# Kernel optimization log

Measured on AMD Instinct MI355X. Metric: run time of the kernel, lower is better.

## Reference

```python
import jax, jax.numpy as jnp
import numpy as np

TAU_M = 2.0   # membrane time constant
TAU_S = 1.0   # synaptic time constant (tau_m = 2*tau_s -> closed-form spike times)
THETA = 1.0   # firing threshold
T_MAX = 20.0  # times beyond this count as 'no spike' (inf)
EPS = 1e-6


def lif_forward(input_spike_times, input_spike_synapse_ids, Wff, Wrec, max_output_spikes):
    """Event-driven recurrent LIF solver.

    PSP kernel: w * (exp(-(t-ts)/TAU_M) - exp(-(t-ts)/TAU_S)).
    Membrane: V(t) = A*z - B*z^2 with z = exp(-t/TAU_M), where A, B accumulate
    w*exp(ts/TAU_M) and w*exp(ts/TAU_S) per processed event. Spike when V = THETA
    (quadratic in z). Reset-by-subtraction of THETA via the membrane kernel.
    Emitted spikes are re-injected through the recurrent weights as new events.
    """
    Bsz, S = input_spike_times.shape
    N = Wff.shape[0]
    M = int(max_output_spikes)
    # process input events in causal (time) order
    order = jnp.argsort(input_spike_times, axis=1)
    t_srt = jnp.take_along_axis(input_spike_times, order, axis=1)
    sid_srt = jnp.take_along_axis(input_spike_synapse_ids, order, axis=1)
    bidx = jnp.arange(Bsz)
    WffT = Wff.T   # (n_synapses, N): row s = weights from synapse s to all neurons
    WrecT = Wrec.T # (N, N): row j = weights from neuron j to all neurons

    def step(carry, _):
        A, Bacc, ptr, t_cur, out_t, out_id, cnt = carry
        ptr_c = jnp.clip(ptr, 0, S - 1)
        t_in = jnp.where(ptr < S, t_srt[bidx, ptr_c], jnp.inf)  # next input event
        sid = sid_srt[bidx, ptr_c]
        # next threshold crossing per neuron: solve A z - B z^2 = THETA
        disc = A * A - 4.0 * THETA * Bacc
        ok_d = (disc > 0.0) & (Bacc > 1e-12)
        sq = jnp.sqrt(jnp.where(ok_d, disc, 1.0))
        Bs = jnp.where(Bacc > 1e-12, Bacc, 1.0)
        z_cur = jnp.exp(-t_cur / TAU_M)[:, None]

        def root_time(z):
            ok = ok_d & (z > 1e-12) & (z < z_cur * (1.0 - EPS))  # strictly in the future
            zs = jnp.where(ok, z, 0.5)
            return jnp.where(ok, -TAU_M * jnp.log(zs), jnp.inf)

        t1 = root_time((A - sq) / (2.0 * Bs))
        t2 = root_time((A + sq) / (2.0 * Bs))
        t_cand = jnp.minimum(t1, t2)                      # (B, N)
        j = jnp.argmin(t_cand, axis=1)                    # earliest-spiking neuron
        t_spk = t_cand[bidx, j]
        emit = (t_spk < t_in) & (t_spk < T_MAX) & (cnt < M)
        consume = (~emit) & jnp.isfinite(t_in)
        any_ev = emit | consume
        t_ev = jnp.where(emit, t_spk, t_in)
        t_evs = jnp.where(any_ev, t_ev, 0.0)
        em = jnp.exp(t_evs / TAU_M)[:, None]
        es = jnp.exp(t_evs / TAU_S)[:, None]
        w_in = WffT[sid]   # (B, N)
        w_rec = WrecT[j]   # (B, N)
        reset = THETA * jax.nn.one_hot(j, N, dtype=A.dtype)
        dA = jnp.where(consume[:, None], w_in * em, 0.0) + jnp.where(emit[:, None], (w_rec - reset) * em, 0.0)
        dB = jnp.where(consume[:, None], w_in * es, 0.0) + jnp.where(emit[:, None], w_rec * es, 0.0)
        A = A + dA
        Bacc = Bacc + dB
        ptr = ptr + consume.astype(ptr.dtype)
        t_cur = jnp.where(any_ev, t_ev, t_cur)
        slot = jnp.clip(cnt, 0, M - 1)
        out_t = out_t.at[bidx, slot].set(jnp.where(emit, t_spk, out_t[bidx, slot]))
        out_id = out_id.at[bidx, slot].set(jnp.where(emit, j.astype(out_id.dtype), out_id[bidx, slot]))
        cnt = cnt + emit.astype(cnt.dtype)
        return (A, Bacc, ptr, t_cur, out_t, out_id, cnt), None

    init = (
        jnp.zeros((Bsz, N), jnp.float32),
        jnp.zeros((Bsz, N), jnp.float32),
        jnp.zeros((Bsz,), jnp.int32),
        jnp.zeros((Bsz,), jnp.float32),
        jnp.full((Bsz, M), jnp.inf, jnp.float32),
        jnp.full((Bsz, M), -1, jnp.int32),
        jnp.zeros((Bsz,), jnp.int32),
    )
    carry, _ = jax.lax.scan(step, init, None, length=S + M)
    return carry[4], carry[5]


def setup_inputs() -> dict:
    key = jax.random.key(0)
    k1, k2, k3, k4 = jax.random.split(key, 4)
    batch, max_in, n_neurons, n_synapses = 256, 256, 128, 256
    input_spike_times = jax.random.uniform(k1, (batch, max_in), dtype=jnp.float32)
    input_spike_synapse_ids = jax.random.randint(k2, (batch, max_in), 0, n_synapses, dtype=jnp.int32)
    # module init: randn + 1.0, rescaled so the membrane operates near threshold
    feedforward_weights = (jax.random.normal(k3, (n_neurons, n_synapses), jnp.float32) + 1.0) * (4.0 / n_synapses)
    recurrent_weights = (jax.random.normal(k4, (n_neurons, n_neurons), jnp.float32) + 1.0) * (1.0 / n_neurons)
    return {
        "input_spike_times": input_spike_times,
        "input_spike_synapse_ids": input_spike_synapse_ids,
        "feedforward_weights": feedforward_weights,
        "recurrent_weights": recurrent_weights,
        "max_output_spikes": 256,
    }


def reference(input_spike_times, input_spike_synapse_ids, feedforward_weights, recurrent_weights, max_output_spikes):
    return lif_forward(input_spike_times, input_spike_synapse_ids, feedforward_weights, recurrent_weights, max_output_spikes)
```

## Files before the change

### kernel.cpp

```cpp
#include <hip/hip_runtime.h>

namespace {

constexpr int BATCH = 256;
constexpr int S_IN  = 256;
constexpr int NNEUR = 128;
constexpr int NSYN  = 256;
constexpr int MOUT  = 256;
constexpr int WSTR  = 130;
constexpr float NO_SPIKE_T = 1.0e30f;
constexpr float K1  = 0.72134752044448170f;
constexpr float NL2 = -1.3862943611198906f;
constexpr float ZEPS = (float)(1.0 - 1e-6);
constexpr float Z20F = 4.5399929762484854e-05f;

constexpr int LDS_WREC  = NNEUR * WSTR * 4;
constexpr int LDS_EV    = LDS_WREC;
constexpr int LDS_SPK   = LDS_EV + 264 * 16;
constexpr int LDS_LT    = LDS_SPK + 264 * 4;
constexpr int LDS_TOTAL = LDS_LT + 1024;

__device__ __forceinline__ float hw_exp2(float x) { return __builtin_amdgcn_exp2f(x); }
__device__ __forceinline__ float hw_log2(float x) { return __builtin_amdgcn_logf(x); }
__device__ __forceinline__ float hw_rcp(float x)  { return __builtin_amdgcn_rcpf(x); }

__global__ void transpose_wff_kernel(const float* __restrict__ wff,
                                     float* __restrict__ wffT) {
    int i = blockIdx.x * blockDim.x + threadIdx.x;
    int s = i >> 7;
    int n = i & (NNEUR - 1);
    wffT[i] = wff[n * NSYN + s];
}

template <int CTRL>
__device__ __forceinline__ int dpp_imax(int v) {
    int t = __builtin_amdgcn_update_dpp(v, v, CTRL, 0xf, 0xf, false);
    return (t > v) ? t : v;
}

__device__ __forceinline__ float cand_z(float A, float B, float zlim) {
    float disc = __builtin_fmaf(A, A, -4.0f * B);
    float r2B  = hw_rcp(B + B);
    float sq   = __fsqrt_rn(disc);
    float z2 = (A + sq) * r2B;
    float z1 = (A - sq) * r2B;
    bool okd = (disc > 0.0f) & (B > 1e-12f);
    bool v2 = okd & (z2 > 1e-12f) & (z2 < zlim);
    bool v1 = okd & (z1 > 1e-12f) & (z1 < zlim);
    return v2 ? z2 : (v1 ? z1 : 0.0f);
}

__global__ __launch_bounds__(64, 1) void lif_event_kernel(
    const float* __restrict__ in_t,
    const int*   __restrict__ in_sid,
    const float* __restrict__ wff,
    const float* __restrict__ wffT,
    const float* __restrict__ wrec,
    int use_t,
    float* __restrict__ out_t,
    float* __restrict__ out_id)
{
    extern __shared__ char smem[];
    float*  wrecL = (float*)smem;
    float4* evL   = (float4*)(smem + LDS_EV);
    int*    spkI  = (int*)  (smem + LDS_SPK);
    float*  lt    = (float*)(smem + LDS_LT);

    const int b = blockIdx.x;
    const int lane = threadIdx.x;

    const float4* wrec4 = (const float4*)wrec;
    for (int i = lane; i < NNEUR * NNEUR / 4; i += 64) {
        float4 v = wrec4[i];
        int n  = i >> 5;
        int c0 = (i & 31) * 4;
        wrecL[(c0 + 0) * WSTR + n] = v.x;
        wrecL[(c0 + 1) * WSTR + n] = v.y;
        wrecL[(c0 + 2) * WSTR + n] = v.z;
        wrecL[(c0 + 3) * WSTR + n] = v.w;
    }

    float myt[4]; int mys[4];
    for (int q = 0; q < 4; ++q) {
        int k = lane + 64 * q;
        myt[q] = in_t[b * S_IN + k];
        mys[q] = in_sid[b * S_IN + k];
        lt[k] = myt[q];
    }
    __syncthreads();
    int rk[4] = {0, 0, 0, 0};
    for (int j = 0; j < S_IN; ++j) {
        float tj = lt[j];
        #pragma unroll
        for (int q = 0; q < 4; ++q)
            rk[q] += (tj < myt[q] || (tj == myt[q] && j < lane + 64 * q)) ? 1 : 0;
    }
    for (int q = 0; q < 4; ++q) {
        float t = myt[q];
        float zi = hw_exp2(-K1 * t);
        float e  = hw_exp2(K1 * t);
        evL[rk[q]] = make_float4(__builtin_bit_cast(float, mys[q]), zi, e, e * e);
    }
    if (lane < 8) evL[S_IN + lane] = make_float4(0.0f, 0.0f, 1.0f, 1.0f);
    __syncthreads();

    const int n0 = lane * 2;
    const int n1 = n0 + 1;
    const int KZ20 = __builtin_bit_cast(int, Z20F) & ~127;

    float A0 = 0.f, A1 = 0.f, B0 = 0.f, B1 = 0.f;
    int ptr = 0, cnt = 0;
    float zlim = ZEPS;

#define LOADW(dst, sid_)                                                     \
    do {                                                                     \
        const int s_ = (sid_);                                               \
        if (use_t) dst = *(const float2*)&wffT[s_ * NNEUR + n0];             \
        else       dst = make_float2(wff[n0 * NSYN + s_], wff[n1 * NSYN + s_]); \
    } while (0)

#define REDUCE_KEY(kk, zc, idxl)                                             \
    do {                                                                     \
        int key_ = (__builtin_bit_cast(int, (zc)) & ~127) | (127 - (idxl));  \
        key_ = dpp_imax<0x111>(key_);                                        \
        key_ = dpp_imax<0x112>(key_);                                        \
        key_ = dpp_imax<0x114>(key_);                                        \
        key_ = dpp_imax<0x118>(key_);                                        \
        key_ = dpp_imax<0x142>(key_);                                        \
        key_ = dpp_imax<0x143>(key_);                                        \
        kk = __builtin_amdgcn_readlane(key_, 63);                            \
    } while (0)

#define APPLY_EMIT(kk)                                                       \
    do {                                                                     \
        const int jn_ = 127 - ((kk) & 127);                                  \
        const float zmax_ = __builtin_bit_cast(float, (kk) & ~127);          \
        const float2 wr_ = *(const float2*)&wrecL[jn_ * WSTR + n0];          \
        const float em_ = hw_rcp(zmax_);                                     \
        const float es_ = em_ * em_;                                         \
        const float r0_ = (n0 == jn_) ? 1.0f : 0.0f;                         \
        const float r1_ = (n1 == jn_) ? 1.0f : 0.0f;                         \
        A0 = __builtin_fmaf(wr_.x - r0_, em_, A0);                           \
        A1 = __builtin_fmaf(wr_.y - r1_, em_, A1);                           \
        B0 = __builtin_fmaf(wr_.x, es_, B0);                                 \
        B1 = __builtin_fmaf(wr_.y, es_, B1);                                 \
        zlim = ZEPS * zmax_;                                                 \
    } while (0)

    float4 evA = evL[0], evB = evL[1], evC = evL[2], evD = evL[3];
    float2 wA, wB, wC, wD;
    LOADW(wA, __builtin_bit_cast(int, evA.x));
    LOADW(wB, __builtin_bit_cast(int, evB.x));
    LOADW(wC, __builtin_bit_cast(int, evC.x));
    LOADW(wD, __builtin_bit_cast(int, evD.x));

    while (ptr + 4 <= S_IN && cnt < MOUT) {
        const float zb0 = cand_z(A0, B0, zlim);
        const float zb1 = cand_z(A1, B1, zlim);
        const float zc = fmaxf(zb0, zb1);
        const int idxl = (zb1 > zb0) ? n1 : n0;
        int key;
        REDUCE_KEY(key, zc, idxl);

        const float A0p = __builtin_fmaf(wA.x, evA.z, A0);
        const float A1p = __builtin_fmaf(wA.y, evA.z, A1);
        const float B0p = __builtin_fmaf(wA.x, evA.w, B0);
        const float B1p = __builtin_fmaf(wA.y, evA.w, B1);
        const float zl1 = ZEPS * evA.y;
        const float zc1 = fmaxf(cand_z(A0p, B0p, zl1), cand_z(A1p, B1p, zl1));

        const float A0q = __builtin_fmaf(wB.x, evB.z, A0p);
        const float A1q = __builtin_fmaf(wB.y, evB.z, A1p);
        const float B0q = __builtin_fmaf(wB.x, evB.w, B0p);
        const float B1q = __builtin_fmaf(wB.y, evB.w, B1p);
        const float zl2 = ZEPS * evB.y;
        const float zc2 = fmaxf(cand_z(A0q, B0q, zl2), cand_z(A1q, B1q, zl2));

        const float A0r = __builtin_fmaf(wC.x, evC.z, A0q);
        const float A1r = __builtin_fmaf(wC.y, evC.z, A1q);
        const float B0r = __builtin_fmaf(wC.x, evC.w, B0q);
        const float B1r = __builtin_fmaf(wC.y, evC.w, B1q);
        const float zl3 = ZEPS * evC.y;
        const float zc3 = fmaxf(cand_z(A0r, B0r, zl3), cand_z(A1r, B1r, zl3));

        const unsigned long long m0 = __ballot((zc  > evA.y) & (zc  > Z20F));
        const unsigned long long m1 = __ballot((zc1 > evB.y) & (zc1 > Z20F));
        const unsigned long long m2 = __ballot((zc2 > evC.y) & (zc2 > Z20F));
        const unsigned long long m3 = __ballot((zc3 > evD.y) & (zc3 > Z20F));

        if (m0 != 0ull) {
            APPLY_EMIT(key);
            if (lane == 0) spkI[cnt] = key;
            ++cnt;
        } else if (m1 != 0ull) {
            A0 = A0p; A1 = A1p; B0 = B0p; B1 = B1p; zlim = zl1; ptr += 1;
            evA = evB; evB = evC; evC = evD; wA = wB; wB = wC; wC = wD;
            evD = evL[ptr + 3];
            LOADW(wD, __builtin_bit_cast(int, evD.x));
        } else if (m2 != 0ull) {
            A0 = A0q; A1 = A1q; B0 = B0q; B1 = B1q; zlim = zl2; ptr += 2;
            evA = evC; evB = evD; wA = wC; wB = wD;
            evC = evL[ptr + 2]; evD = evL[ptr + 3];
            LOADW(wC, __builtin_bit_cast(int, evC.x));
            LOADW(wD, __builtin_bit_cast(int, evD.x));
        } else if (m3 != 0ull) {
            A0 = A0r; A1 = A1r; B0 = B0r; B1 = B1r; zlim = zl3; ptr += 3;
            evA = evD; wA = wD;
            evB = evL[ptr + 1]; evC = evL[ptr + 2]; evD = evL[ptr + 3];
            LOADW(wB, __builtin_bit_cast(int, evB.x));
            LOADW(wC, __builtin_bit_cast(int, evC.x));
            LOADW(wD, __builtin_bit_cast(int, evD.x));
        } else {
            A0 = __builtin_fmaf(wD.x, evD.z, A0r);
            A1 = __builtin_fmaf(wD.y, evD.z, A1r);
            B0 = __builtin_fmaf(wD.x, evD.w, B0r);
            B1 = __builtin_fmaf(wD.y, evD.w, B1r);
            zlim = ZEPS * evD.y; ptr += 4;
            evA = evL[ptr + 0]; evB = evL[ptr + 1];
            evC = evL[ptr + 2]; evD = evL[ptr + 3];
            LOADW(wA, __builtin_bit_cast(int, evA.x));
            LOADW(wB, __builtin_bit_cast(int, evB.x));
            LOADW(wC, __builtin_bit_cast(int, evC.x));
            LOADW(wD, __builtin_bit_cast(int, evD.x));
        }
    }

    while (ptr < S_IN && cnt < MOUT) {
        const float zb0 = cand_z(A0, B0, zlim);
        const float zb1 = cand_z(A1, B1, zlim);
        const float zc = fmaxf(zb0, zb1);
        const int idxl = (zb1 > zb0) ? n1 : n0;
        int key;
        REDUCE_KEY(key, zc, idxl);
        const unsigned long long m = __ballot((zc > evA.y) & (zc > Z20F));
        if (m != 0ull) {
            APPLY_EMIT(key);
            if (lane == 0) spkI[cnt] = key;
            ++cnt;
        } else {
            A0 = __builtin_fmaf(wA.x, evA.z, A0);
            A1 = __builtin_fmaf(wA.y, evA.z, A1);
            B0 = __builtin_fmaf(wA.x, evA.w, B0);
            B1 = __builtin_fmaf(wA.y, evA.w, B1);
            zlim = ZEPS * evA.y;
            ++ptr;
            evA = evB; evB = evC; evC = evD; wA = wB; wB = wC; wC = wD;
            evD = evL[ptr + 3];
            LOADW(wD, __builtin_bit_cast(int, evD.x));
        }
    }

    while (cnt < MOUT) {
        int k0, k1, k2, k3;
        {
            const float zb0 = cand_z(A0, B0, zlim);
            const float zb1 = cand_z(A1, B1, zlim);
            const float zc = fmaxf(zb0, zb1);
            const int idxl = (zb1 > zb0) ? n1 : n0;
            REDUCE_KEY(k0, zc, idxl);
            APPLY_EMIT(k0);
        }
        {
            const float zb0 = cand_z(A0, B0, zlim);
            const float zb1 = cand_z(A1, B1, zlim);
            const float zc = fmaxf(zb0, zb1);
            const int idxl = (zb1 > zb0) ? n1 : n0;
            REDUCE_KEY(k1, zc, idxl);
            APPLY_EMIT(k1);
        }
        {
            const float zb0 = cand_z(A0, B0, zlim);
            const float zb1 = cand_z(A1, B1, zlim);
            const float zc = fmaxf(zb0, zb1);
            const int idxl = (zb1 > zb0) ? n1 : n0;
            REDUCE_KEY(k2, zc, idxl);
            APPLY_EMIT(k2);
        }
        {
            const float zb0 = cand_z(A0, B0, zlim);
            const float zb1 = cand_z(A1, B1, zlim);
            const float zc = fmaxf(zb0, zb1);
            const int idxl = (zb1 > zb0) ? n1 : n0;
            REDUCE_KEY(k3, zc, idxl);
            APPLY_EMIT(k3);
        }
        if (lane == 0) {
            spkI[cnt + 0] = k0; spkI[cnt + 1] = k1;
            spkI[cnt + 2] = k2; spkI[cnt + 3] = k3;
        }
        const bool f0 = (k0 & ~127) <= KZ20;
        const bool f1 = (k1 & ~127) <= KZ20;
        const bool f2 = (k2 & ~127) <= KZ20;
        const bool f3 = (k3 & ~127) <= KZ20;
        const int p = f0 ? 0 : (f1 ? 1 : (f2 ? 2 : (f3 ? 3 : 4)));
        cnt += p;
        if (p < 4) break;
    }
    if (cnt > MOUT) cnt = MOUT;
#undef LOADW
#undef REDUCE_KEY
#undef APPLY_EMIT

    __syncthreads();
    for (int k = lane; k < MOUT; k += 64) {
        const int kk = spkI[k];
        const bool live = (k < cnt);
        const float zmax = __builtin_bit_cast(float, kk & ~127);
        const float t = NL2 * hw_log2(zmax);
        const float id = (float)(127 - (kk & 127));
        out_t[b * MOUT + k]  = live ? t : NO_SPIKE_T;
        out_id[b * MOUT + k] = live ? id : -1.0f;
    }
}

}

extern "C" void kernel_launch(void* const* d_in, const int* in_sizes, int n_in,
                              void* d_out, int out_size, void* d_ws, size_t ws_size,
                              hipStream_t stream) {
    (void)in_sizes; (void)n_in; (void)out_size;
    const float* in_t   = (const float*)d_in[0];
    const int*   in_sid = (const int*)d_in[1];
    const float* wff    = (const float*)d_in[2];
    const float* wrec   = (const float*)d_in[3];

    float* out_t  = (float*)d_out;
    float* out_id = (float*)d_out + BATCH * MOUT;

    float* wffT = (float*)d_ws;
    const size_t need = (size_t)(NSYN * NNEUR) * sizeof(float);
    const int use_t = (ws_size >= need) ? 1 : 0;

    if (use_t) {
        transpose_wff_kernel<<<(NSYN * NNEUR) / 256, 256, 0, stream>>>(wff, wffT);
    }
    lif_event_kernel<<<BATCH, 64, LDS_TOTAL, stream>>>(in_t, in_sid, wff, wffT, wrec,
                                                       use_t, out_t, out_id);
}
```

Before: 163.5 us.

## Pre-bake reset into recurrent weight layout, deepen weight prefetch, unroll emit loop

Stores recurrent weights in LDS as one float4 per lane (reset-adjusted A weights plus B weights), indexed directly by the reduced key, so each emit does a single 16-byte LDS read and no per-neuron reset compare. A separate synapse-id array lets feedforward weight loads be issued eight events ahead instead of four. The key reduction folds both neurons without an extra index select, and the tail emit loop is unrolled to eight steps. LDS use grows to roughly 135 KB and register pressure rises. es is now computed with a second reciprocal, which may differ slightly in rounding from squaring em.

```diff
diff --git a/kernel.cpp b/kernel.cpp
--- a/kernel.cpp
+++ b/kernel.cpp
@@ -7,17 +7,17 @@
 constexpr int NNEUR = 128;
 constexpr int NSYN  = 256;
 constexpr int MOUT  = 256;
-constexpr int WSTR  = 130;
 constexpr float NO_SPIKE_T = 1.0e30f;
 constexpr float K1  = 0.72134752044448170f;
 constexpr float NL2 = -1.3862943611198906f;
 constexpr float ZEPS = (float)(1.0 - 1e-6);
 constexpr float Z20F = 4.5399929762484854e-05f;
 
-constexpr int LDS_WREC  = NNEUR * WSTR * 4;
-constexpr int LDS_EV    = LDS_WREC;
-constexpr int LDS_SPK   = LDS_EV + 264 * 16;
-constexpr int LDS_LT    = LDS_SPK + 264 * 4;
+constexpr int LDS_WR4   = 0;
+constexpr int LDS_EV    = 131072;
+constexpr int LDS_SPK   = LDS_EV + 4224;
+constexpr int LDS_SS    = LDS_SPK + 1056;
+constexpr int LDS_LT    = LDS_SS + 1088;
 constexpr int LDS_TOTAL = LDS_LT + 1024;
 
 __device__ __forceinline__ float hw_exp2(float x) { return __builtin_amdgcn_exp2f(x); }
@@ -61,10 +61,12 @@
     float* __restrict__ out_id)
 {
     extern __shared__ char smem[];
-    float*  wrecL = (float*)smem;
+    float4* wr4   = (float4*)(smem + LDS_WR4);
+    float*  wr4f  = (float*) (smem + LDS_WR4);
     float4* evL   = (float4*)(smem + LDS_EV);
-    int*    spkI  = (int*)  (smem + LDS_SPK);
-    float*  lt    = (float*)(smem + LDS_LT);
+    int*    spkI  = (int*)   (smem + LDS_SPK);
+    int*    ssL   = (int*)   (smem + LDS_SS);
+    float*  lt    = (float*) (smem + LDS_LT);
 
     const int b = blockIdx.x;
     const int lane = threadIdx.x;
@@ -74,10 +76,15 @@
         float4 v = wrec4[i];
         int n  = i >> 5;
         int c0 = (i & 31) * 4;
-        wrecL[(c0 + 0) * WSTR + n] = v.x;
-        wrecL[(c0 + 1) * WSTR + n] = v.y;
-        wrecL[(c0 + 2) * WSTR + n] = v.z;
-        wrecL[(c0 + 3) * WSTR + n] = v.w;
+        int half = n >> 1, comp = n & 1;
+        #pragma unroll
+        for (int q = 0; q < 4; ++q) {
+            int j = c0 + q;
+            float w = (q == 0) ? v.x : (q == 1) ? v.y : (q == 2) ? v.z : v.w;
+            float* cell = &wr4f[((127 - j) * 64 + half) * 4];
+            cell[comp]     = w - ((n == j) ? 1.0f : 0.0f);
+            cell[comp + 2] = w;
+        }
     }
 
     float myt[4]; int mys[4];
@@ -100,8 +107,10 @@
         float zi = hw_exp2(-K1 * t);
         float e  = hw_exp2(K1 * t);
         evL[rk[q]] = make_float4(__builtin_bit_cast(float, mys[q]), zi, e, e * e);
-    }
-    if (lane < 8) evL[S_IN + lane] = make_float4(0.0f, 0.0f, 1.0f, 1.0f);
+        ssL[rk[q]] = mys[q];
+    }
+    if (lane < 8)  evL[S_IN + lane] = make_float4(0.0f, 0.0f, 1.0f, 1.0f);
+    if (lane < 16) ssL[S_IN + lane] = 0;
     __syncthreads();
 
     const int n0 = lane * 2;
@@ -119,9 +128,11 @@
         else       dst = make_float2(wff[n0 * NSYN + s_], wff[n1 * NSYN + s_]); \
     } while (0)
 
-#define REDUCE_KEY(kk, zc, idxl)                                             \
+#define REDUCE_KEY2(kk, zb0_, zb1_)                                          \
     do {                                                                     \
-        int key_ = (__builtin_bit_cast(int, (zc)) & ~127) | (127 - (idxl));  \
+        int ka_ = (__builtin_bit_cast(int, (zb0_)) & ~127) | (127 - n0);     \
+        int kb_ = (__builtin_bit_cast(int, (zb1_)) & ~127) | (127 - n1);     \
+        int key_ = (kb_ > ka_) ? kb_ : ka_;                                  \
         key_ = dpp_imax<0x111>(key_);                                        \
         key_ = dpp_imax<0x112>(key_);                                        \
         key_ = dpp_imax<0x114>(key_);                                        \
@@ -131,97 +142,99 @@
         kk = __builtin_amdgcn_readlane(key_, 63);                            \
     } while (0)
 
-#define APPLY_EMIT(kk)                                                       \
+#define APPLY_EMIT4(kk)                                                      \
     do {                                                                     \
-        const int jn_ = 127 - ((kk) & 127);                                  \
+        const int jr_ = (kk) & 127;                                          \
         const float zmax_ = __builtin_bit_cast(float, (kk) & ~127);          \
-        const float2 wr_ = *(const float2*)&wrecL[jn_ * WSTR + n0];          \
+        const float4 wr_ = wr4[jr_ * 64 + lane];                             \
         const float em_ = hw_rcp(zmax_);                                     \
-        const float es_ = em_ * em_;                                         \
-        const float r0_ = (n0 == jn_) ? 1.0f : 0.0f;                         \
-        const float r1_ = (n1 == jn_) ? 1.0f : 0.0f;                         \
-        A0 = __builtin_fmaf(wr_.x - r0_, em_, A0);                           \
-        A1 = __builtin_fmaf(wr_.y - r1_, em_, A1);                           \
-        B0 = __builtin_fmaf(wr_.x, es_, B0);                                 \
-        B1 = __builtin_fmaf(wr_.y, es_, B1);                                 \
+        const float es_ = hw_rcp(zmax_ * zmax_);                             \
+        A0 = __builtin_fmaf(wr_.x, em_, A0);                                 \
+        A1 = __builtin_fmaf(wr_.y, em_, A1);                                 \
+        B0 = __builtin_fmaf(wr_.z, es_, B0);                                 \
+        B1 = __builtin_fmaf(wr_.w, es_, B1);                                 \
         zlim = ZEPS * zmax_;                                                 \
     } while (0)
 
-    float4 evA = evL[0], evB = evL[1], evC = evL[2], evD = evL[3];
-    float2 wA, wB, wC, wD;
-    LOADW(wA, __builtin_bit_cast(int, evA.x));
-    LOADW(wB, __builtin_bit_cast(int, evB.x));
-    LOADW(wC, __builtin_bit_cast(int, evC.x));
-    LOADW(wD, __builtin_bit_cast(int, evD.x));
+#define EMIT_STEP(kk)                                                        \
+    do {                                                                     \
+        const float zb0_ = cand_z(A0, B0, zlim);                             \
+        const float zb1_ = cand_z(A1, B1, zlim);                             \
+        REDUCE_KEY2(kk, zb0_, zb1_);                                         \
+        APPLY_EMIT4(kk);                                                     \
+    } while (0)
+
+    float4 ev0 = evL[0], ev1 = evL[1], ev2 = evL[2], ev3 = evL[3];
+    float2 w0, w1, w2, w3, w4, w5, w6, w7;
+    LOADW(w0, ssL[0]); LOADW(w1, ssL[1]); LOADW(w2, ssL[2]); LOADW(w3, ssL[3]);
+    LOADW(w4, ssL[4]); LOADW(w5, ssL[5]); LOADW(w6, ssL[6]); LOADW(w7, ssL[7]);
+    int sP0 = ssL[8], sP1 = ssL[9], sP2 = ssL[10], sP3 = ssL[11];
 
     while (ptr + 4 <= S_IN && cnt < MOUT) {
         const float zb0 = cand_z(A0, B0, zlim);
         const float zb1 = cand_z(A1, B1, zlim);
         const float zc = fmaxf(zb0, zb1);
-        const int idxl = (zb1 > zb0) ? n1 : n0;
         int key;
-        REDUCE_KEY(key, zc, idxl);
-
-        const float A0p = __builtin_fmaf(wA.x, evA.z, A0);
-        const float A1p = __builtin_fmaf(wA.y, evA.z, A1);
-        const float B0p = __builtin_fmaf(wA.x, evA.w, B0);
-        const float B1p = __builtin_fmaf(wA.y, evA.w, B1);
-        const float zl1 = ZEPS * evA.y;
+        REDUCE_KEY2(key, zb0, zb1);
+
+        const float A0p = __builtin_fmaf(w0.x, ev0.z, A0);
+        const float A1p = __builtin_fmaf(w0.y, ev0.z, A1);
+        const float B0p = __builtin_fmaf(w0.x, ev0.w, B0);
+        const float B1p = __builtin_fmaf(w0.y, ev0.w, B1);
+        const float zl1 = ZEPS * ev0.y;
         const float zc1 = fmaxf(cand_z(A0p, B0p, zl1), cand_z(A1p, B1p, zl1));
 
-        const float A0q = __builtin_fmaf(wB.x, evB.z, A0p);
-        const float A1q = __builtin_fmaf(wB.y, evB.z, A1p);
-        const float B0q = __builtin_fmaf(wB.x, evB.w, B0p);
-        const float B1q = __builtin_fmaf(wB.y, evB.w, B1p);
-        const float zl2 = ZEPS * evB.y;
+        const float A0q = __builtin_fmaf(w1.x, ev1.z, A0p);
+        const float A1q = __builtin_fmaf(w1.y, ev1.z, A1p);
+        const float B0q = __builtin_fmaf(w1.x, ev1.w, B0p);
+        const float B1q = __builtin_fmaf(w1.y, ev1.w, B1p);
+        const float zl2 = ZEPS * ev1.y;
         const float zc2 = fmaxf(cand_z(A0q, B0q, zl2), cand_z(A1q, B1q, zl2));
 
-        const float A0r = __builtin_fmaf(wC.x, evC.z, A0q);
-        const float A1r = __builtin_fmaf(wC.y, evC.z, A1q);
-        const float B0r = __builtin_fmaf(wC.x, evC.w, B0q);
-        const float B1r = __builtin_fmaf(wC.y, evC.w, B1q);
-        const float zl3 = ZEPS * evC.y;
+        const float A0r = __builtin_fmaf(w2.x, ev2.z, A0q);
+        const float A1r = __builtin_fmaf(w2.y, ev2.z, A1q);
+        const float B0r = __builtin_fmaf(w2.x, ev2.w, B0q);
+        const float B1r = __builtin_fmaf(w2.y, ev2.w, B1q);
+        const float zl3 = ZEPS * ev2.y;
         const float zc3 = fmaxf(cand_z(A0r, B0r, zl3), cand_z(A1r, B1r, zl3));
 
-        const unsigned long long m0 = __ballot((zc  > evA.y) & (zc  > Z20F));
-        const unsigned long long m1 = __ballot((zc1 > evB.y) & (zc1 > Z20F));
-        const unsigned long long m2 = __ballot((zc2 > evC.y) & (zc2 > Z20F));
-        const unsigned long long m3 = __ballot((zc3 > evD.y) & (zc3 > Z20F));
+        const unsigned long long m0 = __ballot((zc  > ev0.y) & (zc  > Z20F));
+        const unsigned long long m1 = __ballot((zc1 > ev1.y) & (zc1 > Z20F));
+        const unsigned long long m2 = __ballot((zc2 > ev2.y) & (zc2 > Z20F));
+        const unsigned long long m3 = __ballot((zc3 > ev3.y) & (zc3 > Z20F));
 
         if (m0 != 0ull) {
-            APPLY_EMIT(key);
+            APPLY_EMIT4(key);
             if (lane == 0) spkI[cnt] = key;
             ++cnt;
         } else if (m1 != 0ull) {
             A0 = A0p; A1 = A1p; B0 = B0p; B1 = B1p; zlim = zl1; ptr += 1;
-            evA = evB; evB = evC; evC = evD; wA = wB; wB = wC; wC = wD;
-            evD = evL[ptr + 3];
-            LOADW(wD, __builtin_bit_cast(int, evD.x));
+            ev0 = ev1; ev1 = ev2; ev2 = ev3; ev3 = evL[ptr + 3];
+            w0 = w1; w1 = w2; w2 = w3; w3 = w4; w4 = w5; w5 = w6; w6 = w7;
+            LOADW(w7, sP0);
+            sP0 = sP1; sP1 = sP2; sP2 = sP3; sP3 = ssL[ptr + 11];
         } else if (m2 != 0ull) {
             A0 = A0q; A1 = A1q; B0 = B0q; B1 = B1q; zlim = zl2; ptr += 2;
-            evA = evC; evB = evD; wA = wC; wB = wD;
-            evC = evL[ptr + 2]; evD = evL[ptr + 3];
-            LOADW(wC, __builtin_bit_cast(int, evC.x));
-            LOADW(wD, __builtin_bit_cast(int, evD.x));
+            ev0 = ev2; ev1 = ev3; ev2 = evL[ptr + 2]; ev3 = evL[ptr + 3];
+            w0 = w2; w1 = w3; w2 = w4; w3 = w5; w4 = w6; w5 = w7;
+            LOADW(w6, sP0); LOADW(w7, sP1);
+            sP0 = sP2; sP1 = sP3; sP2 = ssL[ptr + 10]; sP3 = ssL[ptr + 11];
         } else if (m3 != 0ull) {
             A0 = A0r; A1 = A1r; B0 = B0r; B1 = B1r; zlim = zl3; ptr += 3;
-            evA = evD; wA = wD;
-            evB = evL[ptr + 1]; evC = evL[ptr + 2]; evD = evL[ptr + 3];
-            LOADW(wB, __builtin_bit_cast(int, evB.x));
-            LOADW(wC, __builtin_bit_cast(int, evC.x));
-            LOADW(wD, __builtin_bit_cast(int, evD.x));
+            ev0 = ev3; ev1 = evL[ptr + 1]; ev2 = evL[ptr + 2]; ev3 = evL[ptr + 3];
+            w0 = w3; w1 = w4; w2 = w5; w3 = w6; w4 = w7;
+            LOADW(w5, sP0); LOADW(w6, sP1); LOADW(w7, sP2);
+            sP0 = sP3; sP1 = ssL[ptr + 9]; sP2 = ssL[ptr + 10]; sP3 = ssL[ptr + 11];
         } else {
-            A0 = __builtin_fmaf(wD.x, evD.z, A0r);
-            A1 = __builtin_fmaf(wD.y, evD.z, A1r);
-            B0 = __builtin_fmaf(wD.x, evD.w, B0r);
-            B1 = __builtin_fmaf(wD.y, evD.w, B1r);
-            zlim = ZEPS * evD.y; ptr += 4;
-            evA = evL[ptr + 0]; evB = evL[ptr + 1];
-            evC = evL[ptr + 2]; evD = evL[ptr + 3];
-            LOADW(wA, __builtin_bit_cast(int, evA.x));
-            LOADW(wB, __builtin_bit_cast(int, evB.x));
-            LOADW(wC, __builtin_bit_cast(int, evC.x));
-            LOADW(wD, __builtin_bit_cast(int, evD.x));
+            A0 = __builtin_fmaf(w3.x, ev3.z, A0r);
+            A1 = __builtin_fmaf(w3.y, ev3.z, A1r);
+            B0 = __builtin_fmaf(w3.x, ev3.w, B0r);
+            B1 = __builtin_fmaf(w3.y, ev3.w, B1r);
+            zlim = ZEPS * ev3.y; ptr += 4;
+            ev0 = evL[ptr]; ev1 = evL[ptr + 1]; ev2 = evL[ptr + 2]; ev3 = evL[ptr + 3];
+            w0 = w4; w1 = w5; w2 = w6; w3 = w7;
+            LOADW(w4, sP0); LOADW(w5, sP1); LOADW(w6, sP2); LOADW(w7, sP3);
+            sP0 = ssL[ptr + 8]; sP1 = ssL[ptr + 9]; sP2 = ssL[ptr + 10]; sP3 = ssL[ptr + 11];
         }
     }
 
@@ -229,77 +242,55 @@
         const float zb0 = cand_z(A0, B0, zlim);
         const float zb1 = cand_z(A1, B1, zlim);
         const float zc = fmaxf(zb0, zb1);
-        const int idxl = (zb1 > zb0) ? n1 : n0;
         int key;
-        REDUCE_KEY(key, zc, idxl);
-        const unsigned long long m = __ballot((zc > evA.y) & (zc > Z20F));
+        REDUCE_KEY2(key, zb0, zb1);
+        const unsigned long long m = __ballot((zc > ev0.y) & (zc > Z20F));
         if (m != 0ull) {
-            APPLY_EMIT(key);
+            APPLY_EMIT4(key);
             if (lane == 0) spkI[cnt] = key;
             ++cnt;
         } else {
-            A0 = __builtin_fmaf(wA.x, evA.z, A0);
-            A1 = __builtin_fmaf(wA.y, evA.z, A1);
-            B0 = __builtin_fmaf(wA.x, evA.w, B0);
-            B1 = __builtin_fmaf(wA.y, evA.w, B1);
-            zlim = ZEPS * evA.y;
+            A0 = __builtin_fmaf(w0.x, ev0.z, A0);
+            A1 = __builtin_fmaf(w0.y, ev0.z, A1);
+            B0 = __builtin_fmaf(w0.x, ev0.w, B0);
+            B1 = __builtin_fmaf(w0.y, ev0.w, B1);
+            zlim = ZEPS * ev0.y;
             ++ptr;
-            evA = evB; evB = evC; evC = evD; wA = wB; wB = wC; wC = wD;
-            evD = evL[ptr + 3];
-            LOADW(wD, __builtin_bit_cast(int, evD.x));
+            ev0 = ev1; ev1 = ev2; ev2 = ev3; ev3 = evL[ptr + 3];
+            w0 = w1; w1 = w2; w2 = w3; w3 = w4; w4 = w5; w5 = w6; w6 = w7;
+            LOADW(w7, sP0);
+            sP0 = sP1; sP1 = sP2; sP2 = sP3; sP3 = ssL[ptr + 11];
         }
     }
 
     while (cnt < MOUT) {
-        int k0, k1, k2, k3;
-        {
-            const float zb0 = cand_z(A0, B0, zlim);
-            const float zb1 = cand_z(A1, B1, zlim);
-            const float zc = fmaxf(zb0, zb1);
-            const int idxl = (zb1 > zb0) ? n1 : n0;
-            REDUCE_KEY(k0, zc, idxl);
-            APPLY_EMIT(k0);
-        }
-        {
-            const float zb0 = cand_z(A0, B0, zlim);
-            const float zb1 = cand_z(A1, B1, zlim);
-            const float zc = fmaxf(zb0, zb1);
-            const int idxl = (zb1 > zb0) ? n1 : n0;
-            REDUCE_KEY(k1, zc, idxl);
-            APPLY_EMIT(k1);
-        }
-        {
-            const float zb0 = cand_z(A0, B0, zlim);
-            const float zb1 = cand_z(A1, B1, zlim);
-            const float zc = fmaxf(zb0, zb1);
-            const int idxl = (zb1 > zb0) ? n1 : n0;
-            REDUCE_KEY(k2, zc, idxl);
-            APPLY_EMIT(k2);
-        }
-        {
-            const float zb0 = cand_z(A0, B0, zlim);
-            const float zb1 = cand_z(A1, B1, zlim);
-            const float zc = fmaxf(zb0, zb1);
-            const int idxl = (zb1 > zb0) ? n1 : n0;
-            REDUCE_KEY(k3, zc, idxl);
-            APPLY_EMIT(k3);
-        }
+        int k0, k1, k2, k3, k4, k5, k6, k7;
+        EMIT_STEP(k0); EMIT_STEP(k1); EMIT_STEP(k2); EMIT_STEP(k3);
+        EMIT_STEP(k4); EMIT_STEP(k5); EMIT_STEP(k6); EMIT_STEP(k7);
         if (lane == 0) {
             spkI[cnt + 0] = k0; spkI[cnt + 1] = k1;
             spkI[cnt + 2] = k2; spkI[cnt + 3] = k3;
+            spkI[cnt + 4] = k4; spkI[cnt + 5] = k5;
+            spkI[cnt + 6] = k6; spkI[cnt + 7] = k7;
         }
         const bool f0 = (k0 & ~127) <= KZ20;
         const bool f1 = (k1 & ~127) <= KZ20;
         const bool f2 = (k2 & ~127) <= KZ20;
         const bool f3 = (k3 & ~127) <= KZ20;
-        const int p = f0 ? 0 : (f1 ? 1 : (f2 ? 2 : (f3 ? 3 : 4)));
+        const bool f4 = (k4 & ~127) <= KZ20;
+        const bool f5 = (k5 & ~127) <= KZ20;
+        const bool f6 = (k6 & ~127) <= KZ20;
+        const bool f7 = (k7 & ~127) <= KZ20;
+        const int p = f0 ? 0 : (f1 ? 1 : (f2 ? 2 : (f3 ? 3 :
+                      (f4 ? 4 : (f5 ? 5 : (f6 ? 6 : (f7 ? 7 : 8)))))));
         cnt += p;
-        if (p < 4) break;
+        if (p < 8) break;
     }
     if (cnt > MOUT) cnt = MOUT;
 #undef LOADW
-#undef REDUCE_KEY
-#undef APPLY_EMIT
+#undef REDUCE_KEY2
+#undef APPLY_EMIT4
+#undef EMIT_STEP
 
     __syncthreads();
     for (int k = lane; k < MOUT; k += 64) {
```

After: 181.4 us. 1.11x slower.
